# Kernel tuning notes

Hardware: AMD Instinct MI355X
Metric: run time of the kernel (lower is better)

Reference implementation:

```python
import jax, jax.numpy as jnp
import numpy as np

B, S, D = 4, 2048, 1024
NH, NKV = 16, 4
HD = D // NH  # 64


def _rope(x, freqs):
    # x: [B, H, S, HD], freqs: [B, S, HD//2]
    cos = jnp.concatenate([jnp.cos(freqs), jnp.cos(freqs)], axis=-1)[:, None]  # [B,1,S,HD]
    sin = jnp.concatenate([jnp.sin(freqs), jnp.sin(freqs)], axis=-1)[:, None]
    x1, x2 = x[..., : HD // 2], x[..., HD // 2:]
    rot = jnp.concatenate([-x2, x1], axis=-1)
    return x * cos + rot * sin


def setup_inputs() -> dict:
    key = jax.random.key(0)
    ks = jax.random.split(key, 9)
    return {
        "hidden_states": jax.random.normal(ks[0], (B, S, D), jnp.float32),
        "rotary_pos_emb": jax.random.normal(ks[1], (B, S, HD // 2), jnp.float32),
        "Wq": jax.random.normal(ks[2], (D, NH * HD), jnp.float32) * 0.02,
        "bq": jax.random.normal(ks[3], (NH * HD,), jnp.float32) * 0.02,
        "Wk": jax.random.normal(ks[4], (D, NKV * HD), jnp.float32) * 0.02,
        "bk": jax.random.normal(ks[5], (NKV * HD,), jnp.float32) * 0.02,
        "Wv": jax.random.normal(ks[6], (D, NKV * HD), jnp.float32) * 0.02,
        "bv": jax.random.normal(ks[7], (NKV * HD,), jnp.float32) * 0.02,
        "Wo": jax.random.normal(ks[8], (NH * HD, D), jnp.float32) * 0.02,
    }


def reference(hidden_states, rotary_pos_emb, Wq, bq, Wk, bk, Wv, bv, Wo):
    b, s, _ = hidden_states.shape
    # projections -> [B, H, S, HD]
    q = (hidden_states @ Wq + bq).reshape(b, s, NH, HD).transpose(0, 2, 1, 3)
    k = (hidden_states @ Wk + bk).reshape(b, s, NKV, HD).transpose(0, 2, 1, 3)
    v = (hidden_states @ Wv + bv).reshape(b, s, NKV, HD).transpose(0, 2, 1, 3)
    q = _rope(q, rotary_pos_emb)
    k = _rope(k, rotary_pos_emb)
    groups = NH // NKV
    k = jnp.repeat(k, groups, axis=1)  # [B, NH, S, HD]
    v = jnp.repeat(v, groups, axis=1)
    scaling = HD ** -0.5
    scores = jnp.einsum("bhqd,bhkd->bhqk", q, k) * scaling
    probs = jax.nn.softmax(scores.astype(jnp.float32), axis=-1).astype(q.dtype)
    out = jnp.einsum("bhqk,bhkd->bhqd", probs, v)
    out = out.transpose(0, 2, 1, 3).reshape(b, s, NH * HD)
    return out @ Wo
```

## Files before the change

### kernel.cpp

```cpp
#include <hip/hip_runtime.h>
#include <hip/hip_bf16.h>

#define BB 4
#define SS 2048
#define DD 1024
#define NH 16
#define NKV 4
#define HD 64
#define MROWS (BB*SS)
#define NQKV (NH*HD + 2*NKV*HD)
#define KOFF (NH*HD)

typedef short v8s __attribute__((ext_vector_type(8)));
typedef short v4s __attribute__((ext_vector_type(4)));
typedef float v4f __attribute__((ext_vector_type(4)));
typedef unsigned short u16;
typedef unsigned int u32;

__device__ __forceinline__ float bf2f(u16 u){
  union { float f; u32 i; } x; x.i = ((u32)u) << 16; return x.f;
}
__device__ __forceinline__ u16 f2bf(float f){
  union { __hip_bfloat16 h; u16 u; } x; x.h = __float2bfloat16(f); return x.u;
}
__device__ __forceinline__ u32 cvtpk(float lo, float hi){
  u32 r;
  asm("v_cvt_pk_bf16_f32 %0, %1, %2" : "=v"(r) : "v"(lo), "v"(hi));
  return r;
}
__device__ __forceinline__ v4f vmax4(v4f a, v4f b){
  v4f r;
  #pragma unroll
  for (int j=0;j<4;j++) r[j] = fmaxf(a[j], b[j]);
  return r;
}
__device__ __forceinline__ void gl_lds16(const u16* g, u16* l){
  __builtin_amdgcn_global_load_lds(
      (const __attribute__((address_space(1))) u32*)g,
      (__attribute__((address_space(3))) u32*)l, 16, 0, 0);
}


__global__ void cast_x(const float* __restrict__ in, u16* __restrict__ out, int n4){
  int i = blockIdx.x*256 + threadIdx.x;
  if (i >= n4) return;
  float4 v = reinterpret_cast<const float4*>(in)[i];
  ushort4 o;
  o.x = f2bf(v.x); o.y = f2bf(v.y); o.z = f2bf(v.z); o.w = f2bf(v.w);
  reinterpret_cast<ushort4*>(out)[i] = o;
}

__global__ void build_bqkv(const float* __restrict__ Wq, const float* __restrict__ Wk,
                           const float* __restrict__ Wv, const float* __restrict__ bq,
                           const float* __restrict__ bk, const float* __restrict__ bv,
                           u16* __restrict__ Bt, float* __restrict__ bias){
  int idx = blockIdx.x*256 + threadIdx.x;
  int n = idx >> 10, k = idx & 1023;
  float v;
  if (n < 1024)      v = Wq[k*1024 + n];
  else if (n < 1280) v = Wk[k*256 + (n-1024)];
  else               v = Wv[k*256 + (n-1280)];
  Bt[idx] = f2bf(v);
  if (k == 0) bias[n] = (n < 1024) ? bq[n] : (n < 1280 ? bk[n-1024] : bv[n-1280]);
}

__global__ void build_wo(const float* __restrict__ Wo, u16* __restrict__ Bt){
  int idx = blockIdx.x*256 + threadIdx.x;
  int n = idx >> 10, k = idx & 1023;
  Bt[idx] = f2bf(Wo[k*1024 + n]);
}

__global__ void rope_k(u16* __restrict__ QKV, const float* __restrict__ fr){
  int idx = blockIdx.x*256 + threadIdx.x;
  int d  = idx & 31;
  int hh = (idx >> 5) % 20;
  long row = idx / (20*32);
  int col = (hh < NH) ? hh*HD + d : KOFF + (hh-NH)*HD + d;
  u16* p = QKV + row*NQKV;
  float x1 = bf2f(p[col]);
  float x2 = bf2f(p[col+32]);
  float f = fr[row*32 + d];
  float sn, cs; __sincosf(f, &sn, &cs);
  float sc = (hh < NH) ? 0.125f * 1.44269504088896f : 1.0f;
  p[col]    = f2bf((x1*cs - x2*sn) * sc);
  p[col+32] = f2bf((x2*cs + x1*sn) * sc);
}


template<bool BIAS, typename OT>
__global__ __launch_bounds__(256) void gemm_bt(
    const u16* __restrict__ A, const u16* __restrict__ Bt,
    const float* __restrict__ bias, OT* __restrict__ C,
    int K, int ldc)
{
  __shared__ u16 As[128*32];
  __shared__ u16 Bs[128*32];
  const int tid = threadIdx.x;
  const int wid = tid >> 6, lane = tid & 63;
  const int g = lane >> 4, c = lane & 15;
  const long brow = (long)blockIdx.y * 128;
  const long bcol = (long)blockIdx.x * 128;
  const int wr = (wid >> 1) * 64, wc = (wid & 1) * 64;
  const int srow = tid >> 2;
  const int scol = (tid & 3) * 8;
  const u16* ga = &A [(brow + srow)*K + scol];
  const u16* gb = &Bt[(bcol + srow)*K + scol];
  u16* la = &As[(wid*64)*8];
  u16* lb = &Bs[(wid*64)*8];
  v4f acc[4][4] = {};
  for (int kt = 0; kt < K; kt += 32) {
    __syncthreads();
    gl_lds16(ga + kt,          la);
    gl_lds16(ga + 64*K + kt,   la + 256*8);
    gl_lds16(gb + kt,          lb);
    gl_lds16(gb + 64*K + kt,   lb + 256*8);
    __syncthreads();
    v8s af[4], bf[4];
    #pragma unroll
    for (int m=0;m<4;m++) af[m] = *reinterpret_cast<const v8s*>(&As[(wr + m*16 + c)*32 + g*8]);
    #pragma unroll
    for (int n=0;n<4;n++) bf[n] = *reinterpret_cast<const v8s*>(&Bs[(wc + n*16 + c)*32 + g*8]);
    __builtin_amdgcn_s_setprio(1);
    #pragma unroll
    for (int m=0;m<4;m++)
      #pragma unroll
      for (int n=0;n<4;n++)
        acc[m][n] = __builtin_amdgcn_mfma_f32_16x16x32_bf16(af[m], bf[n], acc[m][n], 0,0,0);
    __builtin_amdgcn_s_setprio(0);
  }
  #pragma unroll
  for (int m=0;m<4;m++)
    #pragma unroll
    for (int n=0;n<4;n++) {
      int col = (int)bcol + wc + n*16 + c;
      float badd = BIAS ? bias[col] : 0.0f;
      #pragma unroll
      for (int r2=0;r2<4;r2++){
        long row = brow + wr + m*16 + g*4 + r2;
        float v = acc[m][n][r2] + badd;
        if constexpr (sizeof(OT)==2) C[row*ldc + col] = (OT)f2bf(v);
        else                         C[row*ldc + col] = (OT)v;
      }
    }
}


__global__ __launch_bounds__(512) void attn_k(const u16* __restrict__ QKV, u16* __restrict__ Out){
  __shared__ u16 Ks[64][72];
  __shared__ u16 Vs[64][72];
  const int tid = threadIdx.x;
  const int wid = tid >> 6, lane = tid & 63;
  const int g = lane >> 4, c = lane & 15;
  const int qt = blockIdx.x & 7;
  const int bh = blockIdx.x >> 3;
  const int b = bh >> 4, h = bh & 15;
  const int kvh = h >> 2;
  const u16* Qb = QKV + (long)b*SS*NQKV + h*HD;
  const u16* Kb = QKV + (long)b*SS*NQKV + KOFF + kvh*HD;
  const u16* Vb = Kb + NKV*HD;

  v8s qf[2][2];
  #pragma unroll
  for (int qn=0;qn<2;qn++)
    #pragma unroll
    for (int ks=0;ks<2;ks++)
      qf[qn][ks] = *reinterpret_cast<const v8s*>(
        &Qb[(long)(qt*256 + wid*32 + qn*16 + c)*NQKV + ks*32 + g*8]);

  v4f o[2][4] = {};
  float mr[2] = {-1e30f, -1e30f};
  float lr[2] = {0.f, 0.f};

  const int krow = tid >> 3;
  const int kcol = (tid & 7) * 8;
  const int key0 = 2*(tid >> 4);
  const int dg4  = (tid & 15) * 4;
  const int slot0 = 32*(key0>>5) + 8*((key0>>2)&3) + 4*((key0>>4)&1) + (key0&3);
  int vofs[4];
  #pragma unroll
  for (int j=0;j<4;j++){
    int d = dg4 + j;
    int idx = (((slot0>>3) ^ (d>>3)) << 3) | (slot0 & 7);
    vofs[j] = d*72 + idx;
  }
  u16* VsF = &Vs[0][0];

  const u16* kp  = Kb + (long)krow*NQKV + kcol;
  const u16* vp0 = Vb + (long)key0*NQKV + dg4;
  const u16* vp1 = vp0 + NQKV;

  v8s kreg; v4s vreg0, vreg1;

  {
    kreg  = *reinterpret_cast<const v8s*>(kp);
    vreg0 = *reinterpret_cast<const v4s*>(vp0);
    vreg1 = *reinterpret_cast<const v4s*>(vp1);
    *reinterpret_cast<v8s*>(&Ks[krow][kcol]) = kreg;
    #pragma unroll
    for (int j=0;j<4;j++)
      *reinterpret_cast<u32*>(&VsF[vofs[j]]) =
        (u32)(u16)vreg0[j] | ((u32)(u16)vreg1[j] << 16);
  }
  __syncthreads();

  for (int t = 0; t < SS/64; ++t){
    if (t+1 < SS/64) {
      long off = (long)(t+1)*64*NQKV;
      kreg  = *reinterpret_cast<const v8s*>(kp  + off);
      vreg0 = *reinterpret_cast<const v4s*>(vp0 + off);
      vreg1 = *reinterpret_cast<const v4s*>(vp1 + off);
    }

    v4f st[4][2] = {};
    #pragma unroll
    for (int ks=0;ks<2;ks++){
      v8s kf[4];
      #pragma unroll
      for (int km=0;km<4;km++)
        kf[km] = *reinterpret_cast<const v8s*>(&Ks[km*16 + c][ks*32 + g*8]);
      __builtin_amdgcn_s_setprio(1);
      #pragma unroll
      for (int km=0;km<4;km++)
        #pragma unroll
        for (int qn=0;qn<2;qn++)
          st[km][qn] = __builtin_amdgcn_mfma_f32_16x16x32_bf16(kf[km], qf[qn][ks], st[km][qn], 0,0,0);
      __builtin_amdgcn_s_setprio(0);
    }

    float al[2];
    bool upd[2];
    #pragma unroll
    for (int qn=0;qn<2;qn++){
      v4f m4 = vmax4(vmax4(st[0][qn], st[1][qn]), vmax4(st[2][qn], st[3][qn]));
      float mx = fmaxf(fmaxf(m4[0], m4[1]), fmaxf(m4[2], m4[3]));
      upd[qn] = !__all(mx <= mr[qn] + 8.0f);
      al[qn] = 1.0f;
      if (upd[qn]) {
        mx = fmaxf(mx, __shfl_xor(mx, 16));
        mx = fmaxf(mx, __shfl_xor(mx, 32));
        float nm = fmaxf(mr[qn], mx);
        float a = __builtin_amdgcn_exp2f(mr[qn] - nm);
        mr[qn] = nm;
        lr[qn] *= a;
        al[qn] = a;
      }
      #pragma unroll
      for (int km=0;km<4;km++)
        #pragma unroll
        for (int r2=0;r2<4;r2++)
          st[km][qn][r2] = __builtin_amdgcn_exp2f(st[km][qn][r2] - mr[qn]);
      v4f s4 = st[0][qn] + st[1][qn] + st[2][qn] + st[3][qn];
      lr[qn] += (s4[0] + s4[1]) + (s4[2] + s4[3]);
    }

    v8s pa[2][2];
    #pragma unroll
    for (int qm=0;qm<2;qm++)
      #pragma unroll
      for (int ks=0;ks<2;ks++){
        union { v8s v; u32 w[4]; } u;
        u.w[0] = cvtpk(st[2*ks  ][qm][0], st[2*ks  ][qm][1]);
        u.w[1] = cvtpk(st[2*ks  ][qm][2], st[2*ks  ][qm][3]);
        u.w[2] = cvtpk(st[2*ks+1][qm][0], st[2*ks+1][qm][1]);
        u.w[3] = cvtpk(st[2*ks+1][qm][2], st[2*ks+1][qm][3]);
        pa[qm][ks] = u.v;
      }

    if (upd[0] | upd[1]) {
      #pragma unroll
      for (int qm=0;qm<2;qm++)
        #pragma unroll
        for (int r2=0;r2<4;r2++){
          float a = __shfl(al[qm], g*4 + r2);
          #pragma unroll
          for (int dn=0;dn<4;dn++) o[qm][dn][r2] *= a;
        }
    }

    #pragma unroll
    for (int ks=0;ks<2;ks++){
      __builtin_amdgcn_s_setprio(1);
      #pragma unroll
      for (int dn=0;dn<4;dn++){
        int d0 = dn*16 + c;
        v8s vf = *reinterpret_cast<const v8s*>(&Vs[d0][(((ks*4+g) ^ (d0>>3)) << 3)]);
        #pragma unroll
        for (int qm=0;qm<2;qm++)
          o[qm][dn] = __builtin_amdgcn_mfma_f32_16x16x32_bf16(pa[qm][ks], vf, o[qm][dn], 0,0,0);
      }
      __builtin_amdgcn_s_setprio(0);
    }

    __syncthreads();
    if (t+1 < SS/64) {
      *reinterpret_cast<v8s*>(&Ks[krow][kcol]) = kreg;
      #pragma unroll
      for (int j=0;j<4;j++)
        *reinterpret_cast<u32*>(&VsF[vofs[j]]) =
          (u32)(u16)vreg0[j] | ((u32)(u16)vreg1[j] << 16);
    }
    __syncthreads();
  }

  #pragma unroll
  for (int qm=0;qm<2;qm++){
    lr[qm] += __shfl_xor(lr[qm], 16);
    lr[qm] += __shfl_xor(lr[qm], 32);
  }
  #pragma unroll
  for (int qm=0;qm<2;qm++)
    #pragma unroll
    for (int r2=0;r2<4;r2++){
      float inv = 1.0f / __shfl(lr[qm], g*4 + r2);
      long row = (long)b*SS + qt*256 + wid*32 + qm*16 + g*4 + r2;
      #pragma unroll
      for (int dn=0;dn<4;dn++)
        Out[row*DD + h*HD + dn*16 + c] = f2bf(o[qm][dn][r2] * inv);
    }
}


extern "C" void kernel_launch(void* const* d_in, const int* in_sizes, int n_in,
                              void* d_out, int out_size, void* d_ws, size_t ws_size,
                              hipStream_t stream)
{
  const float* hs = (const float*)d_in[0];
  const float* fr = (const float*)d_in[1];
  const float* Wq = (const float*)d_in[2];
  const float* bq = (const float*)d_in[3];
  const float* Wk = (const float*)d_in[4];
  const float* bk = (const float*)d_in[5];
  const float* Wv = (const float*)d_in[6];
  const float* bv = (const float*)d_in[7];
  const float* Wo = (const float*)d_in[8];
  float* out = (float*)d_out;
  char* ws = (char*)d_ws;

  u16*   Xb   = (u16*)(ws);
  u16*   Bqkv = (u16*)(ws + 16777216);
  u16*   WoT  = (u16*)(ws + 16777216 + 3145728);
  float* bias = (float*)(ws + 16777216 + 3145728 + 2097152);
  u16*   QKV  = (u16*)(ws + 22028288);
  u16*   AO   = (u16*)(ws + 22028288 + 25165824);

  cast_x   <<<8192, 256, 0, stream>>>(hs, Xb, MROWS*DD/4);
  build_bqkv<<<6144, 256, 0, stream>>>(Wq, Wk, Wv, bq, bk, bv, Bqkv, bias);
  build_wo <<<4096, 256, 0, stream>>>(Wo, WoT);
  gemm_bt<true,  u16>  <<<dim3(NQKV/128, MROWS/128), 256, 0, stream>>>(Xb, Bqkv, bias, QKV, DD, NQKV);
  rope_k   <<<MROWS*20*32/256, 256, 0, stream>>>(QKV, fr);
  attn_k   <<<BB*NH*(SS/256), 512, 0, stream>>>(QKV, AO);
  gemm_bt<false, float><<<dim3(DD/128, MROWS/128), 256, 0, stream>>>(AO, WoT, nullptr, out, DD, DD);
}
```

Measured before the change: 196.4 us.

## Fuse Q RoPE into attention, double-buffer K/V smem, MFMA row-sum

Q rotary embedding and softmax scaling now run in registers inside the attention kernel, so the separate RoPE pass only touches K heads and the Q columns are not read and written an extra time. K/V shared-memory tiles become double-buffered, which removes one of the two barriers per key tile. The softmax denominator is computed with an extra MFMA against a ones vector instead of VALU sums, and V packing uses a byte permute. In exchange it uses twice the shared memory and a fifth accumulator tile, which may affect occupancy, and each attention block recomputes sincos for its Q rows.

```diff
diff --git a/kernel.cpp b/kernel.cpp
--- a/kernel.cpp
+++ b/kernel.cpp
@@ -73,17 +73,16 @@
 __global__ void rope_k(u16* __restrict__ QKV, const float* __restrict__ fr){
   int idx = blockIdx.x*256 + threadIdx.x;
   int d  = idx & 31;
-  int hh = (idx >> 5) % 20;
-  long row = idx / (20*32);
-  int col = (hh < NH) ? hh*HD + d : KOFF + (hh-NH)*HD + d;
+  int hh = (idx >> 5) & 3;
+  long row = idx >> 7;
+  int col = KOFF + hh*HD + d;
   u16* p = QKV + row*NQKV;
   float x1 = bf2f(p[col]);
   float x2 = bf2f(p[col+32]);
   float f = fr[row*32 + d];
   float sn, cs; __sincosf(f, &sn, &cs);
-  float sc = (hh < NH) ? 0.125f * 1.44269504088896f : 1.0f;
-  p[col]    = f2bf((x1*cs - x2*sn) * sc);
-  p[col+32] = f2bf((x2*cs + x1*sn) * sc);
+  p[col]    = f2bf(x1*cs - x2*sn);
+  p[col+32] = f2bf(x2*cs + x1*sn);
 }
 
 
@@ -145,9 +144,11 @@
 }
 
 
-__global__ __launch_bounds__(512) void attn_k(const u16* __restrict__ QKV, u16* __restrict__ Out){
-  __shared__ u16 Ks[64][72];
-  __shared__ u16 Vs[64][72];
+__global__ __launch_bounds__(512) void attn_k(const u16* __restrict__ QKV,
+                                              const float* __restrict__ fr,
+                                              u16* __restrict__ Out){
+  __shared__ u16 Ks[2][64][72];
+  __shared__ u16 Vs[2][64][72];
   const int tid = threadIdx.x;
   const int wid = tid >> 6, lane = tid & 63;
   const int g = lane >> 4, c = lane & 15;
@@ -159,17 +160,43 @@
   const u16* Kb = QKV + (long)b*SS*NQKV + KOFF + kvh*HD;
   const u16* Vb = Kb + NKV*HD;
 
+  const float SCL = 0.125f * 1.44269504088896f;
   v8s qf[2][2];
   #pragma unroll
-  for (int qn=0;qn<2;qn++)
-    #pragma unroll
-    for (int ks=0;ks<2;ks++)
-      qf[qn][ks] = *reinterpret_cast<const v8s*>(
-        &Qb[(long)(qt*256 + wid*32 + qn*16 + c)*NQKV + ks*32 + g*8]);
-
-  v4f o[2][4] = {};
+  for (int qn=0;qn<2;qn++){
+    int lrow = qt*256 + wid*32 + qn*16 + c;
+    v8s q0 = *reinterpret_cast<const v8s*>(&Qb[(long)lrow*NQKV + g*8]);
+    v8s q1 = *reinterpret_cast<const v8s*>(&Qb[(long)lrow*NQKV + 32 + g*8]);
+    const float* frp = fr + ((long)b*SS + lrow)*32 + g*8;
+    float4 f0 = *reinterpret_cast<const float4*>(frp);
+    float4 f1 = *reinterpret_cast<const float4*>(frp + 4);
+    float fa[8] = {f0.x,f0.y,f0.z,f0.w,f1.x,f1.y,f1.z,f1.w};
+    float r0[8], r1[8];
+    #pragma unroll
+    for (int j=0;j<8;j++){
+      float x1 = bf2f((u16)q0[j]), x2 = bf2f((u16)q1[j]);
+      float sn, cs; __sincosf(fa[j], &sn, &cs);
+      r0[j] = (x1*cs - x2*sn) * SCL;
+      r1[j] = (x2*cs + x1*sn) * SCL;
+    }
+    union { v8s v; u32 w[4]; } a0, a1;
+    #pragma unroll
+    for (int wi=0;wi<4;wi++){
+      a0.w[wi] = cvtpk(r0[2*wi], r0[2*wi+1]);
+      a1.w[wi] = cvtpk(r1[2*wi], r1[2*wi+1]);
+    }
+    qf[qn][0] = a0.v; qf[qn][1] = a1.v;
+  }
+
+  v8s onesf;
+  {
+    short ov = (c==0) ? (short)0x3F80 : (short)0;
+    #pragma unroll
+    for (int j=0;j<8;j++) onesf[j] = ov;
+  }
+
+  v4f o[2][5] = {};
   float mr[2] = {-1e30f, -1e30f};
-  float lr[2] = {0.f, 0.f};
 
   const int krow = tid >> 3;
   const int kcol = (tid & 7) * 8;
@@ -183,32 +210,36 @@
     int idx = (((slot0>>3) ^ (d>>3)) << 3) | (slot0 & 7);
     vofs[j] = d*72 + idx;
   }
-  u16* VsF = &Vs[0][0];
+  u16* VsF = &Vs[0][0][0];
 
   const u16* kp  = Kb + (long)krow*NQKV + kcol;
   const u16* vp0 = Vb + (long)key0*NQKV + dg4;
   const u16* vp1 = vp0 + NQKV;
 
-  v8s kreg; v4s vreg0, vreg1;
+  v8s kreg;
+  union { v4s v; u32 w[2]; } vr0, vr1;
 
   {
     kreg  = *reinterpret_cast<const v8s*>(kp);
-    vreg0 = *reinterpret_cast<const v4s*>(vp0);
-    vreg1 = *reinterpret_cast<const v4s*>(vp1);
-    *reinterpret_cast<v8s*>(&Ks[krow][kcol]) = kreg;
-    #pragma unroll
-    for (int j=0;j<4;j++)
-      *reinterpret_cast<u32*>(&VsF[vofs[j]]) =
-        (u32)(u16)vreg0[j] | ((u32)(u16)vreg1[j] << 16);
+    vr0.v = *reinterpret_cast<const v4s*>(vp0);
+    vr1.v = *reinterpret_cast<const v4s*>(vp1);
+    *reinterpret_cast<v8s*>(&Ks[0][krow][kcol]) = kreg;
+    #pragma unroll
+    for (int j=0;j<4;j++){
+      u32 pkd = __builtin_amdgcn_perm(vr1.w[j>>1], vr0.w[j>>1],
+                                      (j&1) ? 0x07060302u : 0x05040100u);
+      *reinterpret_cast<u32*>(&VsF[vofs[j]]) = pkd;
+    }
   }
   __syncthreads();
 
+  int p = 0;
   for (int t = 0; t < SS/64; ++t){
     if (t+1 < SS/64) {
       long off = (long)(t+1)*64*NQKV;
       kreg  = *reinterpret_cast<const v8s*>(kp  + off);
-      vreg0 = *reinterpret_cast<const v4s*>(vp0 + off);
-      vreg1 = *reinterpret_cast<const v4s*>(vp1 + off);
+      vr0.v = *reinterpret_cast<const v4s*>(vp0 + off);
+      vr1.v = *reinterpret_cast<const v4s*>(vp1 + off);
     }
 
     v4f st[4][2] = {};
@@ -217,7 +248,7 @@
       v8s kf[4];
       #pragma unroll
       for (int km=0;km<4;km++)
-        kf[km] = *reinterpret_cast<const v8s*>(&Ks[km*16 + c][ks*32 + g*8]);
+        kf[km] = *reinterpret_cast<const v8s*>(&Ks[p][km*16 + c][ks*32 + g*8]);
       __builtin_amdgcn_s_setprio(1);
       #pragma unroll
       for (int km=0;km<4;km++)
@@ -239,18 +270,14 @@
         mx = fmaxf(mx, __shfl_xor(mx, 16));
         mx = fmaxf(mx, __shfl_xor(mx, 32));
         float nm = fmaxf(mr[qn], mx);
-        float a = __builtin_amdgcn_exp2f(mr[qn] - nm);
+        al[qn] = __builtin_amdgcn_exp2f(mr[qn] - nm);
         mr[qn] = nm;
-        lr[qn] *= a;
-        al[qn] = a;
       }
       #pragma unroll
       for (int km=0;km<4;km++)
         #pragma unroll
         for (int r2=0;r2<4;r2++)
           st[km][qn][r2] = __builtin_amdgcn_exp2f(st[km][qn][r2] - mr[qn]);
-      v4f s4 = st[0][qn] + st[1][qn] + st[2][qn] + st[3][qn];
-      lr[qn] += (s4[0] + s4[1]) + (s4[2] + s4[3]);
     }
 
     v8s pa[2][2];
@@ -273,7 +300,7 @@
         for (int r2=0;r2<4;r2++){
           float a = __shfl(al[qm], g*4 + r2);
           #pragma unroll
-          for (int dn=0;dn<4;dn++) o[qm][dn][r2] *= a;
+          for (int dn=0;dn<5;dn++) o[qm][dn][r2] *= a;
         }
     }
 
@@ -283,35 +310,37 @@
       #pragma unroll
       for (int dn=0;dn<4;dn++){
         int d0 = dn*16 + c;
-        v8s vf = *reinterpret_cast<const v8s*>(&Vs[d0][(((ks*4+g) ^ (d0>>3)) << 3)]);
+        v8s vf = *reinterpret_cast<const v8s*>(&Vs[p][d0][(((ks*4+g) ^ (d0>>3)) << 3)]);
         #pragma unroll
         for (int qm=0;qm<2;qm++)
           o[qm][dn] = __builtin_amdgcn_mfma_f32_16x16x32_bf16(pa[qm][ks], vf, o[qm][dn], 0,0,0);
       }
+      #pragma unroll
+      for (int qm=0;qm<2;qm++)
+        o[qm][4] = __builtin_amdgcn_mfma_f32_16x16x32_bf16(pa[qm][ks], onesf, o[qm][4], 0,0,0);
       __builtin_amdgcn_s_setprio(0);
     }
 
+    if (t+1 < SS/64) {
+      *reinterpret_cast<v8s*>(&Ks[p^1][krow][kcol]) = kreg;
+      const int bofs = (p^1) * (64*72);
+      #pragma unroll
+      for (int j=0;j<4;j++){
+        u32 pkd = __builtin_amdgcn_perm(vr1.w[j>>1], vr0.w[j>>1],
+                                        (j&1) ? 0x07060302u : 0x05040100u);
+        *reinterpret_cast<u32*>(&VsF[bofs + vofs[j]]) = pkd;
+      }
+    }
     __syncthreads();
-    if (t+1 < SS/64) {
-      *reinterpret_cast<v8s*>(&Ks[krow][kcol]) = kreg;
-      #pragma unroll
-      for (int j=0;j<4;j++)
-        *reinterpret_cast<u32*>(&VsF[vofs[j]]) =
-          (u32)(u16)vreg0[j] | ((u32)(u16)vreg1[j] << 16);
-    }
-    __syncthreads();
-  }
-
-  #pragma unroll
-  for (int qm=0;qm<2;qm++){
-    lr[qm] += __shfl_xor(lr[qm], 16);
-    lr[qm] += __shfl_xor(lr[qm], 32);
-  }
+    p ^= 1;
+  }
+
   #pragma unroll
   for (int qm=0;qm<2;qm++)
     #pragma unroll
     for (int r2=0;r2<4;r2++){
-      float inv = 1.0f / __shfl(lr[qm], g*4 + r2);
+      float l = __shfl(o[qm][4][r2], lane & 48);
+      float inv = 1.0f / l;
       long row = (long)b*SS + qt*256 + wid*32 + qm*16 + g*4 + r2;
       #pragma unroll
       for (int dn=0;dn<4;dn++)
@@ -347,7 +376,7 @@
   build_bqkv<<<6144, 256, 0, stream>>>(Wq, Wk, Wv, bq, bk, bv, Bqkv, bias);
   build_wo <<<4096, 256, 0, stream>>>(Wo, WoT);
   gemm_bt<true,  u16>  <<<dim3(NQKV/128, MROWS/128), 256, 0, stream>>>(Xb, Bqkv, bias, QKV, DD, NQKV);
-  rope_k   <<<MROWS*20*32/256, 256, 0, stream>>>(QKV, fr);
-  attn_k   <<<BB*NH*(SS/256), 512, 0, stream>>>(QKV, AO);
+  rope_k   <<<MROWS*NKV*32/256, 256, 0, stream>>>(QKV, fr);
+  attn_k   <<<BB*NH*(SS/256), 512, 0, stream>>>(QKV, fr, AO);
   gemm_bt<false, float><<<dim3(DD/128, MROWS/128), 256, 0, stream>>>(AO, WoT, nullptr, out, DD, DD);
 }
```

Measured after the change: 184.4 us. 6.1% less time.
